# Kernel optimization log

Hardware: AMD Instinct MI355X
Metric: run time of the kernel (lower is better)

Reference implementation:

```python
import jax, jax.numpy as jnp
import numpy as np

HEADS = 4
DIM_HEAD = 128
HIDDEN = HEADS * DIM_HEAD  # 512
DIM = 256
EMBED = 256


def mish(x):
    return x * jnp.tanh(jax.nn.softplus(x))


def setup_inputs() -> dict:
    key = jax.random.key(0)
    k = jax.random.split(key, 7)
    b, a, f, t = 64, 8, DIM, 256
    x = jax.random.normal(k[0], (b, a, f, t), dtype=jnp.float32)
    time = jax.random.normal(k[1], (b, a, EMBED), dtype=jnp.float32)
    # to_qkv: Conv2d(dim, 3*hidden, 1, bias=False) -> weight [3*hidden, dim]
    w_qkv = jax.random.normal(k[2], (3 * HIDDEN, DIM), dtype=jnp.float32) * (1.0 / np.sqrt(DIM))
    # time_mlp: Mish -> Linear(embed, 3*hidden)
    w_time = jax.random.normal(k[3], (3 * HIDDEN, EMBED), dtype=jnp.float32) * (1.0 / np.sqrt(EMBED))
    b_time = jax.random.normal(k[4], (3 * HIDDEN,), dtype=jnp.float32) * 0.01
    # to_out: Conv2d(hidden, dim, 1) with bias
    w_out = jax.random.normal(k[5], (DIM, HIDDEN), dtype=jnp.float32) * (1.0 / np.sqrt(HIDDEN))
    b_out = jax.random.normal(k[6], (DIM,), dtype=jnp.float32) * 0.01
    return {"x": x, "time": time, "w_qkv": w_qkv, "w_time": w_time,
            "b_time": b_time, "w_out": w_out, "b_out": b_out}


def reference(x, time, w_qkv, w_time, b_time, w_out, b_out):
    b, a, f, t = x.shape
    heads, c = HEADS, DIM_HEAD
    # x: b a f t -> b f a t (channels-first for 1x1 conv)
    xp = jnp.transpose(x, (0, 2, 1, 3))  # [b, f, a, t]
    # 1x1 conv == channel GEMM
    qkv = jnp.einsum('of,bfat->boat', w_qkv, xp)  # [b, 3*hidden, a, t]
    # time MLP: Mish -> Linear; bias broadcast over t
    temb = mish(time) @ w_time.T + b_time          # [b, a, 3*hidden]
    temb = jnp.transpose(temb, (0, 2, 1))[..., None]  # [b, 3*hidden, a, 1]
    qkv = qkv + temb
    # 'b (qkv heads c) h w -> qkv (b h) heads c w' with h=a, w=t
    qkv = qkv.reshape(b, 3, heads, c, a, t)
    qkv = jnp.transpose(qkv, (1, 0, 4, 2, 3, 5)).reshape(3, b * a, heads, c, t)
    q, k, v = qkv[0], qkv[1], qkv[2]  # each [(b a), heads, c, t]
    k = jax.nn.softmax(k, axis=-1)
    # linear attention: context over keys/values, then apply to q
    context = jnp.einsum('bhdn,bhen->bhde', k, v)   # [(b a), heads, c, c]
    out = jnp.einsum('bhde,bhdn->bhen', context, q)  # [(b a), heads, c, t]
    # '(b h) heads c w -> b (heads c) h w'
    out = out.reshape(b, a, heads * c, t)
    out = jnp.transpose(out, (0, 2, 1, 3))  # [b, hidden, a, t]
    out = jnp.einsum('of,bfat->boat', w_out, out) + b_out[None, :, None, None]
    # b f a t -> b a f t
    return jnp.transpose(out, (0, 2, 1, 3))
```

## Files before the change

### kernel.cpp

```cpp
#include <hip/hip_runtime.h>

typedef __bf16 bf16;
typedef __bf16 bf16x4 __attribute__((ext_vector_type(4)));
typedef __bf16 bf16x8 __attribute__((ext_vector_type(8)));
typedef float  f32x4  __attribute__((ext_vector_type(4)));

#define TT    256
#define FF    256
#define SG    256
#define NGRP  2

static __device__ inline f32x4 mfma16(bf16x8 a, bf16x8 b, f32x4 c) {
    return __builtin_amdgcn_mfma_f32_16x16x32_bf16(a, b, c, 0, 0, 0);
}

typedef const __attribute__((address_space(1))) unsigned int* gp_t;
typedef __attribute__((address_space(3))) unsigned int* lp_t;
static __device__ inline void gll16(const bf16* g, bf16* l) {
    __builtin_amdgcn_global_load_lds((gp_t)g, (lp_t)l, 16, 0, 0);
}

static __device__ inline void stage128g(const bf16* __restrict__ g, int ld, bf16* __restrict__ l) {
    int lane = threadIdx.x & 63, wv = threadIdx.x >> 6;
    int r = lane >> 2, c8 = (lane & 3) * 8;
#pragma unroll
    for (int i = 0; i < 2; i++) {
        int row0 = wv * 32 + i * 16;
        gll16(g + (size_t)(row0 + r) * ld + c8, l + row0 * 32);
    }
}
static __device__ inline void stage256g(const bf16* __restrict__ g, int ld, bf16* __restrict__ l) {
    int lane = threadIdx.x & 63, wv = threadIdx.x >> 6;
    int r = lane >> 2, c8 = (lane & 3) * 8;
#pragma unroll
    for (int i = 0; i < 4; i++) {
        int row0 = wv * 64 + i * 16;
        gll16(g + (size_t)(row0 + r) * ld + c8, l + row0 * 32);
    }
}
static __device__ inline bf16x8 fragld(const bf16* __restrict__ l, int row0) {
    int lane = threadIdx.x & 63;
    return *(const bf16x8*)(l + (row0 + (lane & 15)) * 32 + (lane >> 4) * 8);
}
static __device__ inline bf16x8 fragld_s(const bf16* __restrict__ l, int row0, int stride) {
    int lane = threadIdx.x & 63;
    return *(const bf16x8*)(l + (row0 + (lane & 15)) * stride + (lane >> 4) * 8);
}

__global__ __launch_bounds__(256) void k_cvt(const float4* __restrict__ src, bf16* __restrict__ dst) {
    int i = blockIdx.x * 256 + threadIdx.x;
    float4 v = src[i];
    bf16x4 o;
    o[0] = (__bf16)v.x; o[1] = (__bf16)v.y; o[2] = (__bf16)v.z; o[3] = (__bf16)v.w;
    *(bf16x4*)(dst + (size_t)i * 4) = o;
}

__global__ __launch_bounds__(256) void k_mish(const float4* __restrict__ src, bf16* __restrict__ dst) {
    int i = blockIdx.x * 256 + threadIdx.x;
    float4 v = src[i];
    float in[4] = {v.x, v.y, v.z, v.w};
    bf16x4 o;
#pragma unroll
    for (int j = 0; j < 4; j++) {
        float sp = log1pf(__expf(in[j]));
        o[j] = (__bf16)(in[j] * tanhf(sp));
    }
    *(bf16x4*)(dst + (size_t)i * 4) = o;
}

__global__ __launch_bounds__(256) void k_xpose(const float* __restrict__ x, bf16* __restrict__ xT) {
    __shared__ float tile[64][65];
    int bid = blockIdx.x;
    int s  = bid >> 4;
    int f0 = ((bid >> 2) & 3) * 64;
    int t0 = (bid & 3) * 64;
    int tid = threadIdx.x;
    int rr = tid >> 4;
    int cc = (tid & 15) * 4;
    const float* xp = x + ((size_t)(s * FF + f0)) * TT + t0;
#pragma unroll
    for (int i = 0; i < 4; i++) {
        int r = i * 16 + rr;
        float4 v = *(const float4*)(xp + (size_t)r * TT + cc);
        tile[r][cc] = v.x; tile[r][cc + 1] = v.y; tile[r][cc + 2] = v.z; tile[r][cc + 3] = v.w;
    }
    __syncthreads();
    bf16* op = xT + ((size_t)(s * TT + t0)) * FF + f0;
#pragma unroll
    for (int i = 0; i < 4; i++) {
        int tr = i * 16 + rr;
        bf16x4 o;
        o[0] = (__bf16)tile[cc][tr];     o[1] = (__bf16)tile[cc + 1][tr];
        o[2] = (__bf16)tile[cc + 2][tr]; o[3] = (__bf16)tile[cc + 3][tr];
        *(bf16x4*)(op + (size_t)tr * FF + cc) = o;
    }
}

__global__ __launch_bounds__(256) void k_temb(const bf16* __restrict__ wt, const bf16* __restrict__ mish,
                                              const float* __restrict__ bt, float* __restrict__ tembT) {
    __shared__ bf16 lA[128 * 32];
    __shared__ bf16 lB[128 * 32];
    int o0 = blockIdx.x * 128, s0 = blockIdx.y * 128;
    int tid = threadIdx.x, wv = tid >> 6, lane = tid & 63, qd = lane >> 4, c = lane & 15;
    f32x4 acc[2][8] = {};
    for (int k0 = 0; k0 < 256; k0 += 32) {
        __syncthreads();
        stage128g(wt + (size_t)o0 * 256 + k0, 256, lA);
        stage128g(mish + (size_t)s0 * 256 + k0, 256, lB);
        __syncthreads();
        bf16x8 a0 = fragld(lA, wv * 32), a1 = fragld(lA, wv * 32 + 16);
#pragma unroll
        for (int nt = 0; nt < 8; nt++) {
            bf16x8 b = fragld(lB, nt * 16);
            acc[0][nt] = mfma16(a0, b, acc[0][nt]);
            acc[1][nt] = mfma16(a1, b, acc[1][nt]);
        }
    }
#pragma unroll
    for (int mt = 0; mt < 2; mt++)
#pragma unroll
        for (int nt = 0; nt < 8; nt++)
#pragma unroll
            for (int r = 0; r < 4; r++) {
                int o = o0 + wv * 32 + mt * 16 + qd * 4 + r;
                int s = s0 + nt * 16 + c;
                tembT[(size_t)o * 512 + s] = acc[mt][nt][r] + bt[o];
            }
}

__global__ __launch_bounds__(256) void k_qkv(const bf16* __restrict__ wq, const bf16* __restrict__ xT,
                                             const float* __restrict__ tembT,
                                             bf16* __restrict__ qt, bf16* __restrict__ kk, bf16* __restrict__ vv) {
    __shared__ bf16 lA[128 * 32];
    __shared__ bf16 lB[128 * 32];
    int b = blockIdx.x;
    int w = (b & 7) * (24 * SG / 8) + (b >> 3);
    int s = w / 24, j = w - s * 24;
    int oc = j >> 1, th = j & 1;
    int o0 = oc * 128, t0 = th * 128;
    int tid = threadIdx.x, wv = tid >> 6, lane = tid & 63, qd = lane >> 4, c = lane & 15;
    const bf16* xs = xT + (size_t)s * (TT * FF) + (size_t)t0 * FF;
    f32x4 acc[2][8] = {};
    for (int k0 = 0; k0 < 256; k0 += 32) {
        __syncthreads();
        stage128g(wq + (size_t)o0 * 256 + k0, 256, lA);
        stage128g(xs + k0, 256, lB);
        __syncthreads();
        bf16x8 a0 = fragld(lA, wv * 32), a1 = fragld(lA, wv * 32 + 16);
#pragma unroll
        for (int nt = 0; nt < 8; nt++) {
            bf16x8 bfr = fragld(lB, nt * 16);
            acc[0][nt] = mfma16(a0, bfr, acc[0][nt]);
            acc[1][nt] = mfma16(a1, bfr, acc[1][nt]);
        }
    }
    int sec = oc >> 2, h = oc & 3;
    float tb[2][4];
#pragma unroll
    for (int mt = 0; mt < 2; mt++)
#pragma unroll
        for (int r = 0; r < 4; r++)
            tb[mt][r] = tembT[(size_t)(o0 + wv * 32 + mt * 16 + qd * 4 + r) * 512 + s];
    if (sec == 0) {
#pragma unroll
        for (int mt = 0; mt < 2; mt++)
#pragma unroll
            for (int nt = 0; nt < 8; nt++) {
                int t = t0 + nt * 16 + c, dl = wv * 32 + mt * 16 + qd * 4;
                bf16x4 o;
#pragma unroll
                for (int r = 0; r < 4; r++) o[r] = (__bf16)(acc[mt][nt][r] + tb[mt][r]);
                *(bf16x4*)(qt + (((size_t)s * 4 + h) * 256 + t) * 128 + dl) = o;
            }
    } else {
        bf16* dst0 = (sec == 1 ? kk : vv);
#pragma unroll
        for (int mt = 0; mt < 2; mt++)
#pragma unroll
            for (int nt = 0; nt < 8; nt++) {
                int t = t0 + nt * 16 + c, dl = wv * 32 + mt * 16 + qd * 4;
                bf16* d = dst0 + (((size_t)s * 4 + h) * 128 + dl) * 256 + t;
#pragma unroll
                for (int r = 0; r < 4; r++) d[(size_t)r * 256] = (__bf16)(acc[mt][nt][r] + tb[mt][r]);
            }
    }
}

__global__ __launch_bounds__(256) void k_attn(const bf16* __restrict__ kk, const bf16* __restrict__ vv,
                                              const bf16* __restrict__ qt, bf16* __restrict__ midT) {
    __shared__ __align__(16) char smem[52224];
    float* mx = (float*)smem;
    float* rs = mx + 128;
    bf16* lA  = (bf16*)(smem + 1024);
    bf16* lB  = (bf16*)(smem + 1024 + 8192);
    bf16* lQ  = (bf16*)(smem + 1024);
    bf16* lct = (bf16*)(smem + 1024 + 16384);
    int bid = blockIdx.x;
    int s = bid >> 2, h = bid & 3;
    size_t base = ((size_t)s * 4 + h) * 32768;
    const bf16* kb = kk + base;
    const bf16* vb = vv + base;
    int tid = threadIdx.x, wv = tid >> 6, lane = tid & 63, qd = lane >> 4, c = lane & 15;

    {
        int d = tid >> 1, half = tid & 1;
        const bf16* p = kb + (size_t)d * 256 + half * 128;
        float m = -3e38f, l = 0.f;
#pragma unroll
        for (int ci = 0; ci < 16; ci++) {
            bf16x8 v8 = *(const bf16x8*)(p + ci * 8);
            float xv[8]; float cm = -3e38f;
#pragma unroll
            for (int j = 0; j < 8; j++) { xv[j] = (float)v8[j]; cm = fmaxf(cm, xv[j]); }
            if (cm > m) { l *= __expf(m - cm); m = cm; }
#pragma unroll
            for (int j = 0; j < 8; j++) l += __expf(xv[j] - m);
        }
        float mo = __shfl_xor(m, 1);
        float lo = __shfl_xor(l, 1);
        float M = fmaxf(m, mo);
        float L = l * __expf(m - M) + lo * __expf(mo - M);
        if (half == 0) { mx[d] = M; rs[d] = 1.0f / L; }
    }
    __syncthreads();

    f32x4 cacc[2][8] = {};
    for (int k0 = 0; k0 < 256; k0 += 32) {
        __syncthreads();
        stage128g(vb + k0, 256, lA);
        stage128g(kb + k0, 256, lB);
        __syncthreads();
        bf16x8 a0 = fragld(lA, wv * 32), a1 = fragld(lA, wv * 32 + 16);
#pragma unroll
        for (int nt = 0; nt < 8; nt++) {
            bf16x8 kf = fragld(lB, nt * 16);
            float md = mx[nt * 16 + c];
            bf16x8 b;
#pragma unroll
            for (int j = 0; j < 8; j++) b[j] = (__bf16)__expf((float)kf[j] - md);
            cacc[0][nt] = mfma16(a0, b, cacc[0][nt]);
            cacc[1][nt] = mfma16(a1, b, cacc[1][nt]);
        }
    }
    __syncthreads();
#pragma unroll
    for (int mt = 0; mt < 2; mt++)
#pragma unroll
        for (int nt = 0; nt < 8; nt++) {
            int d = nt * 16 + c;
            float rv = rs[d];
#pragma unroll
            for (int r = 0; r < 4; r++) {
                int e = wv * 32 + mt * 16 + qd * 4 + r;
                lct[e * 136 + d] = (__bf16)(cacc[mt][nt][r] * rv);
            }
        }
    __syncthreads();
    const bf16* qb = qt + base;
    for (int th = 0; th < 2; th++) {
        f32x4 oacc[2][8] = {};
        for (int d0 = 0; d0 < 128; d0 += 32) {
            __syncthreads();
            stage128g(qb + (size_t)th * 128 * 128 + d0, 128, lQ);
            __syncthreads();
            bf16x8 a0 = fragld_s(lct + d0, wv * 32, 136), a1 = fragld_s(lct + d0, wv * 32 + 16, 136);
#pragma unroll
            for (int nt = 0; nt < 8; nt++) {
                bf16x8 qf = fragld(lQ, nt * 16);
                oacc[0][nt] = mfma16(a0, qf, oacc[0][nt]);
                oacc[1][nt] = mfma16(a1, qf, oacc[1][nt]);
            }
        }
#pragma unroll
        for (int mt = 0; mt < 2; mt++)
#pragma unroll
            for (int nt = 0; nt < 8; nt++) {
                int t = th * 128 + nt * 16 + c;
                int e = wv * 32 + mt * 16 + qd * 4;
                bf16x4 o;
#pragma unroll
                for (int r = 0; r < 4; r++) o[r] = (__bf16)oacc[mt][nt][r];
                *(bf16x4*)(midT + ((size_t)s * 256 + t) * 512 + h * 128 + e) = o;
            }
    }
}

__global__ __launch_bounds__(256) void k_out(const bf16* __restrict__ wo, const bf16* __restrict__ midT,
                                             const float* __restrict__ bo, float* __restrict__ y) {
    __shared__ bf16 lA[128 * 32];
    __shared__ bf16 lB[128 * 32];
    int b = blockIdx.x;
    int w = (b & 7) * (4 * SG / 8) + (b >> 3);
    int s = w >> 2, j = w & 3;
    int o0 = (j >> 1) * 128, t0 = (j & 1) * 128;
    int tid = threadIdx.x, wv = tid >> 6, lane = tid & 63, qd = lane >> 4, c = lane & 15;
    const bf16* ms = midT + (size_t)s * 131072 + (size_t)t0 * 512;
    f32x4 acc[2][8] = {};
    for (int k0 = 0; k0 < 512; k0 += 32) {
        __syncthreads();
        stage128g(wo + (size_t)o0 * 512 + k0, 512, lA);
        stage128g(ms + k0, 512, lB);
        __syncthreads();
        bf16x8 a0 = fragld(lA, wv * 32), a1 = fragld(lA, wv * 32 + 16);
#pragma unroll
        for (int nt = 0; nt < 8; nt++) {
            bf16x8 bfr = fragld(lB, nt * 16);
            acc[0][nt] = mfma16(a0, bfr, acc[0][nt]);
            acc[1][nt] = mfma16(a1, bfr, acc[1][nt]);
        }
    }
    float bb[2][4];
#pragma unroll
    for (int mt = 0; mt < 2; mt++)
#pragma unroll
        for (int r = 0; r < 4; r++)
            bb[mt][r] = bo[o0 + wv * 32 + mt * 16 + qd * 4 + r];
#pragma unroll
    for (int mt = 0; mt < 2; mt++)
#pragma unroll
        for (int nt = 0; nt < 8; nt++)
#pragma unroll
            for (int r = 0; r < 4; r++) {
                int o = o0 + wv * 32 + mt * 16 + qd * 4 + r;
                int t = t0 + nt * 16 + c;
                y[((size_t)(s * 256 + o)) * 256 + t] = acc[mt][nt][r] + bb[mt][r];
            }
}

extern "C" void kernel_launch(void* const* d_in, const int* in_sizes, int n_in,
                              void* d_out, int out_size, void* d_ws, size_t ws_size,
                              hipStream_t stream) {
    const float* x      = (const float*)d_in[0];
    const float* time_  = (const float*)d_in[1];
    const float* w_qkv  = (const float*)d_in[2];
    const float* w_time = (const float*)d_in[3];
    const float* b_time = (const float*)d_in[4];
    const float* w_out  = (const float*)d_in[5];
    const float* b_out  = (const float*)d_in[6];
    float* y = (float*)d_out;
    char* ws = (char*)d_ws;

    bf16*  wqkv_bf  = (bf16*)(ws + 0);
    bf16*  wtime_bf = (bf16*)(ws + 786432);
    bf16*  wout_bf  = (bf16*)(ws + 1572864);
    bf16*  mish_bf  = (bf16*)(ws + 1835008);
    float* tembT    = (float*)(ws + 2097152);
    bf16*  qt       = (bf16*)(ws + 5242880);
    bf16*  kk       = (bf16*)(ws + 72351744);
    bf16*  vv       = (bf16*)(ws + 139460608);
    bf16*  midT     = (bf16*)(ws + 206569472);
    bf16*  xT       = (bf16*)(ws + 206569472);

    k_cvt<<<384, 256, 0, stream>>>((const float4*)w_qkv, wqkv_bf);
    k_cvt<<<384, 256, 0, stream>>>((const float4*)w_time, wtime_bf);
    k_cvt<<<128, 256, 0, stream>>>((const float4*)w_out, wout_bf);
    k_mish<<<128, 256, 0, stream>>>((const float4*)time_, mish_bf);
    k_temb<<<dim3(12, 4), 256, 0, stream>>>(wtime_bf, mish_bf, b_time, tembT);

    for (int g = 0; g < NGRP; g++) {
        const float* xg = x + (size_t)g * SG * FF * TT;
        float*       yg = y + (size_t)g * SG * 256 * TT;
        const float* tg = tembT + (size_t)g * SG;
        k_xpose<<<SG * 16, 256, 0, stream>>>(xg, xT);
        k_qkv<<<24 * SG, 256, 0, stream>>>(wqkv_bf, xT, tg, qt, kk, vv);
        k_attn<<<SG * 4, 256, 0, stream>>>(kk, vv, qt, midT);
        k_out<<<4 * SG, 256, 0, stream>>>(wout_bf, midT, b_out, yg);
    }
}
```

Measured before the change: 634.7 us.

## Double-buffer LDS tiles to overlap global loads with MFMA in all GEMMs

Converts the single-buffered LDS staging in k_temb, k_qkv, k_attn and k_out to ping-pong buffers. The next K-slice is issued with global_load_lds before computing on the current one. This leaves one barrier per iteration instead of two and hides load latency behind MFMA work. In k_attn the first V/K tiles are prefetched during the softmax-statistics pass, and Q tiles are prefetched across the th/d0 loops. The cost is doubled LDS per block (k_attn grows to about 67 KB), which can reduce how many blocks fit on a CU. The unused stage256g helper is removed.

```diff
diff --git a/kernel.cpp b/kernel.cpp
--- a/kernel.cpp
+++ b/kernel.cpp
@@ -26,15 +26,6 @@
 #pragma unroll
     for (int i = 0; i < 2; i++) {
         int row0 = wv * 32 + i * 16;
-        gll16(g + (size_t)(row0 + r) * ld + c8, l + row0 * 32);
-    }
-}
-static __device__ inline void stage256g(const bf16* __restrict__ g, int ld, bf16* __restrict__ l) {
-    int lane = threadIdx.x & 63, wv = threadIdx.x >> 6;
-    int r = lane >> 2, c8 = (lane & 3) * 8;
-#pragma unroll
-    for (int i = 0; i < 4; i++) {
-        int row0 = wv * 64 + i * 16;
         gll16(g + (size_t)(row0 + r) * ld + c8, l + row0 * 32);
     }
 }
@@ -98,23 +89,29 @@
 
 __global__ __launch_bounds__(256) void k_temb(const bf16* __restrict__ wt, const bf16* __restrict__ mish,
                                               const float* __restrict__ bt, float* __restrict__ tembT) {
-    __shared__ bf16 lA[128 * 32];
-    __shared__ bf16 lB[128 * 32];
+    __shared__ bf16 lA[2][128 * 32];
+    __shared__ bf16 lB[2][128 * 32];
     int o0 = blockIdx.x * 128, s0 = blockIdx.y * 128;
     int tid = threadIdx.x, wv = tid >> 6, lane = tid & 63, qd = lane >> 4, c = lane & 15;
     f32x4 acc[2][8] = {};
+    stage128g(wt + (size_t)o0 * 256, 256, lA[0]);
+    stage128g(mish + (size_t)s0 * 256, 256, lB[0]);
+    __syncthreads();
+    int cur = 0;
     for (int k0 = 0; k0 < 256; k0 += 32) {
-        __syncthreads();
-        stage128g(wt + (size_t)o0 * 256 + k0, 256, lA);
-        stage128g(mish + (size_t)s0 * 256 + k0, 256, lB);
-        __syncthreads();
-        bf16x8 a0 = fragld(lA, wv * 32), a1 = fragld(lA, wv * 32 + 16);
-#pragma unroll
-        for (int nt = 0; nt < 8; nt++) {
-            bf16x8 b = fragld(lB, nt * 16);
+        if (k0 + 32 < 256) {
+            stage128g(wt + (size_t)o0 * 256 + k0 + 32, 256, lA[cur ^ 1]);
+            stage128g(mish + (size_t)s0 * 256 + k0 + 32, 256, lB[cur ^ 1]);
+        }
+        bf16x8 a0 = fragld(lA[cur], wv * 32), a1 = fragld(lA[cur], wv * 32 + 16);
+#pragma unroll
+        for (int nt = 0; nt < 8; nt++) {
+            bf16x8 b = fragld(lB[cur], nt * 16);
             acc[0][nt] = mfma16(a0, b, acc[0][nt]);
             acc[1][nt] = mfma16(a1, b, acc[1][nt]);
         }
+        __syncthreads();
+        cur ^= 1;
     }
 #pragma unroll
     for (int mt = 0; mt < 2; mt++)
@@ -131,8 +128,8 @@
 __global__ __launch_bounds__(256) void k_qkv(const bf16* __restrict__ wq, const bf16* __restrict__ xT,
                                              const float* __restrict__ tembT,
                                              bf16* __restrict__ qt, bf16* __restrict__ kk, bf16* __restrict__ vv) {
-    __shared__ bf16 lA[128 * 32];
-    __shared__ bf16 lB[128 * 32];
+    __shared__ bf16 lA[2][128 * 32];
+    __shared__ bf16 lB[2][128 * 32];
     int b = blockIdx.x;
     int w = (b & 7) * (24 * SG / 8) + (b >> 3);
     int s = w / 24, j = w - s * 24;
@@ -141,18 +138,24 @@
     int tid = threadIdx.x, wv = tid >> 6, lane = tid & 63, qd = lane >> 4, c = lane & 15;
     const bf16* xs = xT + (size_t)s * (TT * FF) + (size_t)t0 * FF;
     f32x4 acc[2][8] = {};
+    stage128g(wq + (size_t)o0 * 256, 256, lA[0]);
+    stage128g(xs, 256, lB[0]);
+    __syncthreads();
+    int cur = 0;
     for (int k0 = 0; k0 < 256; k0 += 32) {
-        __syncthreads();
-        stage128g(wq + (size_t)o0 * 256 + k0, 256, lA);
-        stage128g(xs + k0, 256, lB);
-        __syncthreads();
-        bf16x8 a0 = fragld(lA, wv * 32), a1 = fragld(lA, wv * 32 + 16);
-#pragma unroll
-        for (int nt = 0; nt < 8; nt++) {
-            bf16x8 bfr = fragld(lB, nt * 16);
+        if (k0 + 32 < 256) {
+            stage128g(wq + (size_t)o0 * 256 + k0 + 32, 256, lA[cur ^ 1]);
+            stage128g(xs + k0 + 32, 256, lB[cur ^ 1]);
+        }
+        bf16x8 a0 = fragld(lA[cur], wv * 32), a1 = fragld(lA[cur], wv * 32 + 16);
+#pragma unroll
+        for (int nt = 0; nt < 8; nt++) {
+            bf16x8 bfr = fragld(lB[cur], nt * 16);
             acc[0][nt] = mfma16(a0, bfr, acc[0][nt]);
             acc[1][nt] = mfma16(a1, bfr, acc[1][nt]);
         }
+        __syncthreads();
+        cur ^= 1;
     }
     int sec = oc >> 2, h = oc & 3;
     float tb[2][4];
@@ -186,15 +189,15 @@
     }
 }
 
+#define SM_LA2(i) ((bf16*)(smem + 1024 + (size_t)(i) * 8192))
+#define SM_LB2(i) ((bf16*)(smem + 1024 + 16384 + (size_t)(i) * 8192))
+#define SM_LQ(i)  ((bf16*)(smem + 1024 + (size_t)(i) * 8192))
 __global__ __launch_bounds__(256) void k_attn(const bf16* __restrict__ kk, const bf16* __restrict__ vv,
                                               const bf16* __restrict__ qt, bf16* __restrict__ midT) {
-    __shared__ __align__(16) char smem[52224];
+    __shared__ __align__(16) char smem[68608];
     float* mx = (float*)smem;
     float* rs = mx + 128;
-    bf16* lA  = (bf16*)(smem + 1024);
-    bf16* lB  = (bf16*)(smem + 1024 + 8192);
-    bf16* lQ  = (bf16*)(smem + 1024);
-    bf16* lct = (bf16*)(smem + 1024 + 16384);
+    bf16* lct = (bf16*)(smem + 1024 + 32768);
     int bid = blockIdx.x;
     int s = bid >> 2, h = bid & 3;
     size_t base = ((size_t)s * 4 + h) * 32768;
@@ -202,6 +205,9 @@
     const bf16* vb = vv + base;
     int tid = threadIdx.x, wv = tid >> 6, lane = tid & 63, qd = lane >> 4, c = lane & 15;
 
+    stage128g(vb, 256, SM_LA2(0));
+    stage128g(kb, 256, SM_LB2(0));
+
     {
         int d = tid >> 1, half = tid & 1;
         const bf16* p = kb + (size_t)d * 256 + half * 128;
@@ -225,15 +231,16 @@
     __syncthreads();
 
     f32x4 cacc[2][8] = {};
+    int cur = 0;
     for (int k0 = 0; k0 < 256; k0 += 32) {
-        __syncthreads();
-        stage128g(vb + k0, 256, lA);
-        stage128g(kb + k0, 256, lB);
-        __syncthreads();
-        bf16x8 a0 = fragld(lA, wv * 32), a1 = fragld(lA, wv * 32 + 16);
-#pragma unroll
-        for (int nt = 0; nt < 8; nt++) {
-            bf16x8 kf = fragld(lB, nt * 16);
+        if (k0 + 32 < 256) {
+            stage128g(vb + k0 + 32, 256, SM_LA2(cur ^ 1));
+            stage128g(kb + k0 + 32, 256, SM_LB2(cur ^ 1));
+        }
+        bf16x8 a0 = fragld(SM_LA2(cur), wv * 32), a1 = fragld(SM_LA2(cur), wv * 32 + 16);
+#pragma unroll
+        for (int nt = 0; nt < 8; nt++) {
+            bf16x8 kf = fragld(SM_LB2(cur), nt * 16);
             float md = mx[nt * 16 + c];
             bf16x8 b;
 #pragma unroll
@@ -241,8 +248,13 @@
             cacc[0][nt] = mfma16(a0, b, cacc[0][nt]);
             cacc[1][nt] = mfma16(a1, b, cacc[1][nt]);
         }
-    }
-    __syncthreads();
+        __syncthreads();
+        cur ^= 1;
+    }
+
+    const bf16* qb = qt + base;
+    stage128g(qb, 128, SM_LQ(0));
+
 #pragma unroll
     for (int mt = 0; mt < 2; mt++)
 #pragma unroll
@@ -256,20 +268,25 @@
             }
         }
     __syncthreads();
-    const bf16* qb = qt + base;
+
+    cur = 0;
     for (int th = 0; th < 2; th++) {
         f32x4 oacc[2][8] = {};
         for (int d0 = 0; d0 < 128; d0 += 32) {
-            __syncthreads();
-            stage128g(qb + (size_t)th * 128 * 128 + d0, 128, lQ);
-            __syncthreads();
+            int idx = th * 4 + (d0 >> 5);
+            if (idx < 7) {
+                int n = idx + 1, th2 = n >> 2, d02 = (n & 3) * 32;
+                stage128g(qb + (size_t)th2 * 128 * 128 + d02, 128, SM_LQ(cur ^ 1));
+            }
             bf16x8 a0 = fragld_s(lct + d0, wv * 32, 136), a1 = fragld_s(lct + d0, wv * 32 + 16, 136);
 #pragma unroll
             for (int nt = 0; nt < 8; nt++) {
-                bf16x8 qf = fragld(lQ, nt * 16);
+                bf16x8 qf = fragld(SM_LQ(cur), nt * 16);
                 oacc[0][nt] = mfma16(a0, qf, oacc[0][nt]);
                 oacc[1][nt] = mfma16(a1, qf, oacc[1][nt]);
             }
+            __syncthreads();
+            cur ^= 1;
         }
 #pragma unroll
         for (int mt = 0; mt < 2; mt++)
@@ -287,8 +304,8 @@
 
 __global__ __launch_bounds__(256) void k_out(const bf16* __restrict__ wo, const bf16* __restrict__ midT,
                                              const float* __restrict__ bo, float* __restrict__ y) {
-    __shared__ bf16 lA[128 * 32];
-    __shared__ bf16 lB[128 * 32];
+    __shared__ bf16 lA[2][128 * 32];
+    __shared__ bf16 lB[2][128 * 32];
     int b = blockIdx.x;
     int w = (b & 7) * (4 * SG / 8) + (b >> 3);
     int s = w >> 2, j = w & 3;
@@ -296,18 +313,24 @@
     int tid = threadIdx.x, wv = tid >> 6, lane = tid & 63, qd = lane >> 4, c = lane & 15;
     const bf16* ms = midT + (size_t)s * 131072 + (size_t)t0 * 512;
     f32x4 acc[2][8] = {};
+    stage128g(wo + (size_t)o0 * 512, 512, lA[0]);
+    stage128g(ms, 512, lB[0]);
+    __syncthreads();
+    int cur = 0;
     for (int k0 = 0; k0 < 512; k0 += 32) {
-        __syncthreads();
-        stage128g(wo + (size_t)o0 * 512 + k0, 512, lA);
-        stage128g(ms + k0, 512, lB);
-        __syncthreads();
-        bf16x8 a0 = fragld(lA, wv * 32), a1 = fragld(lA, wv * 32 + 16);
-#pragma unroll
-        for (int nt = 0; nt < 8; nt++) {
-            bf16x8 bfr = fragld(lB, nt * 16);
+        if (k0 + 32 < 512) {
+            stage128g(wo + (size_t)o0 * 512 + k0 + 32, 512, lA[cur ^ 1]);
+            stage128g(ms + k0 + 32, 512, lB[cur ^ 1]);
+        }
+        bf16x8 a0 = fragld(lA[cur], wv * 32), a1 = fragld(lA[cur], wv * 32 + 16);
+#pragma unroll
+        for (int nt = 0; nt < 8; nt++) {
+            bf16x8 bfr = fragld(lB[cur], nt * 16);
             acc[0][nt] = mfma16(a0, bfr, acc[0][nt]);
             acc[1][nt] = mfma16(a1, bfr, acc[1][nt]);
         }
+        __syncthreads();
+        cur ^= 1;
     }
     float bb[2][4];
 #pragma unroll
```

Result: no change. 646.8 us (+1.9%).

## Double-buffer LDS staging with async global_load_lds prefetch in GEMM kernels

Applied to the files above, without the earlier changes.

Converts the K-loops of the qkv, attention and output kernels from single-buffered LDS staging with two __syncthreads per step into a two-stage ping-pong pipeline. Tiles for step t+2 are issued with global_load_lds right after step t is consumed, and each step waits on partial vmcnt counts. The goal is to hide global-load latency behind MFMA work. In the attention kernel, the first K/V tiles are also prefetched during the softmax-stats pass, and the Q tiles are prefetched while the context is written to LDS. The cost is more LDS per block, which can lower occupancy, and hand-tuned waitcnt values that are fragile if the load counts change.

```diff
diff --git a/kernel.cpp b/kernel.cpp
--- a/kernel.cpp
+++ b/kernel.cpp
@@ -10,6 +10,11 @@
 #define SG    256
 #define NGRP  2
 
+#define SCHED0 __builtin_amdgcn_sched_barrier(0)
+#define BAR    __builtin_amdgcn_s_barrier()
+#define WAITVM(N) asm volatile("s_waitcnt vmcnt(" #N ")" ::: "memory")
+#define WAITLGKM0 asm volatile("s_waitcnt lgkmcnt(0)" ::: "memory")
+
 static __device__ inline f32x4 mfma16(bf16x8 a, bf16x8 b, f32x4 c) {
     return __builtin_amdgcn_mfma_f32_16x16x32_bf16(a, b, c, 0, 0, 0);
 }
@@ -26,15 +31,6 @@
 #pragma unroll
     for (int i = 0; i < 2; i++) {
         int row0 = wv * 32 + i * 16;
-        gll16(g + (size_t)(row0 + r) * ld + c8, l + row0 * 32);
-    }
-}
-static __device__ inline void stage256g(const bf16* __restrict__ g, int ld, bf16* __restrict__ l) {
-    int lane = threadIdx.x & 63, wv = threadIdx.x >> 6;
-    int r = lane >> 2, c8 = (lane & 3) * 8;
-#pragma unroll
-    for (int i = 0; i < 4; i++) {
-        int row0 = wv * 64 + i * 16;
         gll16(g + (size_t)(row0 + r) * ld + c8, l + row0 * 32);
     }
 }
@@ -131,28 +127,40 @@
 __global__ __launch_bounds__(256) void k_qkv(const bf16* __restrict__ wq, const bf16* __restrict__ xT,
                                              const float* __restrict__ tembT,
                                              bf16* __restrict__ qt, bf16* __restrict__ kk, bf16* __restrict__ vv) {
-    __shared__ bf16 lA[128 * 32];
-    __shared__ bf16 lB[128 * 32];
+    __shared__ bf16 lA[2][128 * 32];
+    __shared__ bf16 lB[2][128 * 32];
     int b = blockIdx.x;
     int w = (b & 7) * (24 * SG / 8) + (b >> 3);
     int s = w / 24, j = w - s * 24;
     int oc = j >> 1, th = j & 1;
     int o0 = oc * 128, t0 = th * 128;
     int tid = threadIdx.x, wv = tid >> 6, lane = tid & 63, qd = lane >> 4, c = lane & 15;
+    const bf16* wA = wq + (size_t)o0 * 256;
     const bf16* xs = xT + (size_t)s * (TT * FF) + (size_t)t0 * FF;
     f32x4 acc[2][8] = {};
-    for (int k0 = 0; k0 < 256; k0 += 32) {
-        __syncthreads();
-        stage128g(wq + (size_t)o0 * 256 + k0, 256, lA);
-        stage128g(xs + k0, 256, lB);
-        __syncthreads();
-        bf16x8 a0 = fragld(lA, wv * 32), a1 = fragld(lA, wv * 32 + 16);
+    stage128g(wA, 256, lA[0]);
+    stage128g(xs, 256, lB[0]);
+    SCHED0;
+    stage128g(wA + 32, 256, lA[1]);
+    stage128g(xs + 32, 256, lB[1]);
+    SCHED0;
+#pragma unroll
+    for (int t = 0; t < 8; t++) {
+        if (t == 7) { WAITVM(0); } else { WAITVM(4); }
+        SCHED0; BAR; SCHED0;
+        bf16x8 a0 = fragld(lA[t & 1], wv * 32), a1 = fragld(lA[t & 1], wv * 32 + 16);
 #pragma unroll
         for (int nt = 0; nt < 8; nt++) {
-            bf16x8 bfr = fragld(lB, nt * 16);
+            bf16x8 bfr = fragld(lB[t & 1], nt * 16);
             acc[0][nt] = mfma16(a0, bfr, acc[0][nt]);
             acc[1][nt] = mfma16(a1, bfr, acc[1][nt]);
         }
+        SCHED0; BAR; SCHED0;
+        if (t + 2 < 8) {
+            stage128g(wA + (t + 2) * 32, 256, lA[t & 1]);
+            stage128g(xs + (t + 2) * 32, 256, lB[t & 1]);
+        }
+        SCHED0;
     }
     int sec = oc >> 2, h = oc & 3;
     float tb[2][4];
@@ -186,15 +194,15 @@
     }
 }
 
+#define SM_LA2(i) ((bf16*)(smem + 1024 + (size_t)(i) * 8192))
+#define SM_LB2(i) ((bf16*)(smem + 1024 + 16384 + (size_t)(i) * 8192))
+#define SM_LQ(i)  ((bf16*)(smem + 1024 + (size_t)(i) * 8192))
 __global__ __launch_bounds__(256) void k_attn(const bf16* __restrict__ kk, const bf16* __restrict__ vv,
                                               const bf16* __restrict__ qt, bf16* __restrict__ midT) {
-    __shared__ __align__(16) char smem[52224];
+    __shared__ __align__(16) char smem[68608];
     float* mx = (float*)smem;
     float* rs = mx + 128;
-    bf16* lA  = (bf16*)(smem + 1024);
-    bf16* lB  = (bf16*)(smem + 1024 + 8192);
-    bf16* lQ  = (bf16*)(smem + 1024);
-    bf16* lct = (bf16*)(smem + 1024 + 16384);
+    bf16* lct = (bf16*)(smem + 1024 + 32768);
     int bid = blockIdx.x;
     int s = bid >> 2, h = bid & 3;
     size_t base = ((size_t)s * 4 + h) * 32768;
@@ -202,6 +210,13 @@
     const bf16* vb = vv + base;
     int tid = threadIdx.x, wv = tid >> 6, lane = tid & 63, qd = lane >> 4, c = lane & 15;
 
+    stage128g(vb, 256, SM_LA2(0));
+    stage128g(kb, 256, SM_LB2(0));
+    SCHED0;
+    stage128g(vb + 32, 256, SM_LA2(1));
+    stage128g(kb + 32, 256, SM_LB2(1));
+    SCHED0;
+
     {
         int d = tid >> 1, half = tid & 1;
         const bf16* p = kb + (size_t)d * 256 + half * 128;
@@ -225,24 +240,35 @@
     __syncthreads();
 
     f32x4 cacc[2][8] = {};
-    for (int k0 = 0; k0 < 256; k0 += 32) {
-        __syncthreads();
-        stage128g(vb + k0, 256, lA);
-        stage128g(kb + k0, 256, lB);
-        __syncthreads();
-        bf16x8 a0 = fragld(lA, wv * 32), a1 = fragld(lA, wv * 32 + 16);
+#pragma unroll
+    for (int t = 0; t < 8; t++) {
+        if (t == 7) { WAITVM(0); } else { WAITVM(4); }
+        SCHED0; BAR; SCHED0;
+        bf16x8 a0 = fragld(SM_LA2(t & 1), wv * 32), a1 = fragld(SM_LA2(t & 1), wv * 32 + 16);
 #pragma unroll
         for (int nt = 0; nt < 8; nt++) {
-            bf16x8 kf = fragld(lB, nt * 16);
+            bf16x8 kf = fragld(SM_LB2(t & 1), nt * 16);
             float md = mx[nt * 16 + c];
-            bf16x8 b;
-#pragma unroll
-            for (int j = 0; j < 8; j++) b[j] = (__bf16)__expf((float)kf[j] - md);
-            cacc[0][nt] = mfma16(a0, b, cacc[0][nt]);
-            cacc[1][nt] = mfma16(a1, b, cacc[1][nt]);
-        }
-    }
-    __syncthreads();
+            bf16x8 bb;
+#pragma unroll
+            for (int j = 0; j < 8; j++) bb[j] = (__bf16)__expf((float)kf[j] - md);
+            cacc[0][nt] = mfma16(a0, bb, cacc[0][nt]);
+            cacc[1][nt] = mfma16(a1, bb, cacc[1][nt]);
+        }
+        SCHED0; BAR; SCHED0;
+        if (t + 2 < 8) {
+            stage128g(vb + (t + 2) * 32, 256, SM_LA2(t & 1));
+            stage128g(kb + (t + 2) * 32, 256, SM_LB2(t & 1));
+        }
+        SCHED0;
+    }
+
+    const bf16* qb = qt + base;
+    stage128g(qb, 128, SM_LQ(0));
+    SCHED0;
+    stage128g(qb + 32, 128, SM_LQ(1));
+    SCHED0;
+
 #pragma unroll
     for (int mt = 0; mt < 2; mt++)
 #pragma unroll
@@ -255,21 +281,33 @@
                 lct[e * 136 + d] = (__bf16)(cacc[mt][nt][r] * rv);
             }
         }
-    __syncthreads();
-    const bf16* qb = qt + base;
+    WAITLGKM0;
+    SCHED0; BAR; SCHED0;
+
+#pragma unroll
     for (int th = 0; th < 2; th++) {
         f32x4 oacc[2][8] = {};
-        for (int d0 = 0; d0 < 128; d0 += 32) {
-            __syncthreads();
-            stage128g(qb + (size_t)th * 128 * 128 + d0, 128, lQ);
-            __syncthreads();
+#pragma unroll
+        for (int dd = 0; dd < 4; dd++) {
+            int idx = th * 4 + dd;
+            int d0 = dd * 32;
+            if (idx == 7)                    { WAITVM(0); }
+            else if (idx == 4 || idx == 5)   { WAITVM(16); }
+            else                             { WAITVM(2); }
+            SCHED0; BAR; SCHED0;
             bf16x8 a0 = fragld_s(lct + d0, wv * 32, 136), a1 = fragld_s(lct + d0, wv * 32 + 16, 136);
 #pragma unroll
             for (int nt = 0; nt < 8; nt++) {
-                bf16x8 qf = fragld(lQ, nt * 16);
+                bf16x8 qf = fragld(SM_LQ(idx & 1), nt * 16);
                 oacc[0][nt] = mfma16(a0, qf, oacc[0][nt]);
                 oacc[1][nt] = mfma16(a1, qf, oacc[1][nt]);
             }
+            SCHED0; BAR; SCHED0;
+            if (idx + 2 < 8) {
+                int n = idx + 2;
+                stage128g(qb + (size_t)(n >> 2) * 16384 + (n & 3) * 32, 128, SM_LQ(idx & 1));
+            }
+            SCHED0;
         }
 #pragma unroll
         for (int mt = 0; mt < 2; mt++)
@@ -287,27 +325,39 @@
 
 __global__ __launch_bounds__(256) void k_out(const bf16* __restrict__ wo, const bf16* __restrict__ midT,
                                              const float* __restrict__ bo, float* __restrict__ y) {
-    __shared__ bf16 lA[128 * 32];
-    __shared__ bf16 lB[128 * 32];
+    __shared__ bf16 lA[2][128 * 32];
+    __shared__ bf16 lB[2][128 * 32];
     int b = blockIdx.x;
     int w = (b & 7) * (4 * SG / 8) + (b >> 3);
     int s = w >> 2, j = w & 3;
     int o0 = (j >> 1) * 128, t0 = (j & 1) * 128;
     int tid = threadIdx.x, wv = tid >> 6, lane = tid & 63, qd = lane >> 4, c = lane & 15;
+    const bf16* wA = wo + (size_t)o0 * 512;
     const bf16* ms = midT + (size_t)s * 131072 + (size_t)t0 * 512;
     f32x4 acc[2][8] = {};
-    for (int k0 = 0; k0 < 512; k0 += 32) {
-        __syncthreads();
-        stage128g(wo + (size_t)o0 * 512 + k0, 512, lA);
-        stage128g(ms + k0, 512, lB);
-        __syncthreads();
-        bf16x8 a0 = fragld(lA, wv * 32), a1 = fragld(lA, wv * 32 + 16);
+    stage128g(wA, 512, lA[0]);
+    stage128g(ms, 512, lB[0]);
+    SCHED0;
+    stage128g(wA + 32, 512, lA[1]);
+    stage128g(ms + 32, 512, lB[1]);
+    SCHED0;
+#pragma unroll
+    for (int t = 0; t < 16; t++) {
+        if (t == 15) { WAITVM(0); } else { WAITVM(4); }
+        SCHED0; BAR; SCHED0;
+        bf16x8 a0 = fragld(lA[t & 1], wv * 32), a1 = fragld(lA[t & 1], wv * 32 + 16);
 #pragma unroll
         for (int nt = 0; nt < 8; nt++) {
-            bf16x8 bfr = fragld(lB, nt * 16);
+            bf16x8 bfr = fragld(lB[t & 1], nt * 16);
             acc[0][nt] = mfma16(a0, bfr, acc[0][nt]);
             acc[1][nt] = mfma16(a1, bfr, acc[1][nt]);
         }
+        SCHED0; BAR; SCHED0;
+        if (t + 2 < 16) {
+            stage128g(wA + (t + 2) * 32, 512, lA[t & 1]);
+            stage128g(ms + (t + 2) * 32, 512, lB[t & 1]);
+        }
+        SCHED0;
     }
     float bb[2][4];
 #pragma unroll
```

After: 616.6 us. 2.9% less time.

## Fuse QKV projection with linear attention and double-buffer output GEMM

Applied to the files above, without the earlier changes.

Merges the QKV projection and attention kernels into one 512-thread kernel per (sample, head). It computes K and V per 128-token half into LDS, runs an online softmax across the halves, then recomputes Q and applies the context, so the large q/k/v intermediates never go to global memory. The output projection GEMM also gains double-buffered LDS staging with explicit vmcnt waits. The costs are a large LDS footprint that limits occupancy, only 1024 blocks for the fused kernel, and x being reloaded for the Q pass.

```diff
diff --git a/kernel.cpp b/kernel.cpp
--- a/kernel.cpp
+++ b/kernel.cpp
@@ -10,6 +10,10 @@
 #define SG    256
 #define NGRP  2
 
+#define SCHED0 __builtin_amdgcn_sched_barrier(0)
+#define BAR    __builtin_amdgcn_s_barrier()
+#define WAITVM(N) asm volatile("s_waitcnt vmcnt(" #N ")" ::: "memory")
+
 static __device__ inline f32x4 mfma16(bf16x8 a, bf16x8 b, f32x4 c) {
     return __builtin_amdgcn_mfma_f32_16x16x32_bf16(a, b, c, 0, 0, 0);
 }
@@ -29,14 +33,11 @@
         gll16(g + (size_t)(row0 + r) * ld + c8, l + row0 * 32);
     }
 }
-static __device__ inline void stage256g(const bf16* __restrict__ g, int ld, bf16* __restrict__ l) {
+static __device__ inline void stage8(const bf16* __restrict__ g, int ld, bf16* __restrict__ l) {
     int lane = threadIdx.x & 63, wv = threadIdx.x >> 6;
     int r = lane >> 2, c8 = (lane & 3) * 8;
-#pragma unroll
-    for (int i = 0; i < 4; i++) {
-        int row0 = wv * 64 + i * 16;
-        gll16(g + (size_t)(row0 + r) * ld + c8, l + row0 * 32);
-    }
+    int row0 = wv * 16;
+    gll16(g + (size_t)(row0 + r) * ld + c8, l + row0 * 32);
 }
 static __device__ inline bf16x8 fragld(const bf16* __restrict__ l, int row0) {
     int lane = threadIdx.x & 63;
@@ -128,186 +129,218 @@
             }
 }
 
-__global__ __launch_bounds__(256) void k_qkv(const bf16* __restrict__ wq, const bf16* __restrict__ xT,
-                                             const float* __restrict__ tembT,
-                                             bf16* __restrict__ qt, bf16* __restrict__ kk, bf16* __restrict__ vv) {
-    __shared__ bf16 lA[128 * 32];
-    __shared__ bf16 lB[128 * 32];
+__global__ __launch_bounds__(512) void k_fused(const bf16* __restrict__ wqkv, const bf16* __restrict__ xT,
+                                               const float* __restrict__ tembT, bf16* __restrict__ midT) {
+    __shared__ __align__(16) char smem[124928];
+    bf16*  lx  = (bf16*)(smem);
+    bf16*  lwA = (bf16*)(smem + 8192);
+    bf16*  lwB = (bf16*)(smem + 16384);
+    float* mx  = (float*)(smem + 24576);
+    float* ls  = (float*)(smem + 25088);
+    float* rs  = (float*)(smem + 25600);
+    float* rfb = (float*)(smem + 26112);
+    bf16*  lk  = (bf16*)(smem + 26624);
+    bf16*  lv  = (bf16*)(smem + 59392);
+    bf16*  lq  = (bf16*)(smem + 92160);
+    bf16*  lct = (bf16*)(smem + 26624);
+
     int b = blockIdx.x;
-    int w = (b & 7) * (24 * SG / 8) + (b >> 3);
-    int s = w / 24, j = w - s * 24;
-    int oc = j >> 1, th = j & 1;
-    int o0 = oc * 128, t0 = th * 128;
+    int w = (b & 7) * (4 * SG / 8) + (b >> 3);
+    int s = w >> 2, h = w & 3;
     int tid = threadIdx.x, wv = tid >> 6, lane = tid & 63, qd = lane >> 4, c = lane & 15;
-    const bf16* xs = xT + (size_t)s * (TT * FF) + (size_t)t0 * FF;
-    f32x4 acc[2][8] = {};
-    for (int k0 = 0; k0 < 256; k0 += 32) {
-        __syncthreads();
-        stage128g(wq + (size_t)o0 * 256 + k0, 256, lA);
-        stage128g(xs + k0, 256, lB);
-        __syncthreads();
-        bf16x8 a0 = fragld(lA, wv * 32), a1 = fragld(lA, wv * 32 + 16);
+    const bf16* xs = xT + (size_t)s * (TT * FF);
+    const bf16* Wq = wqkv + (size_t)(h * 128) * 256;
+    const bf16* Wk = wqkv + (size_t)(512 + h * 128) * 256;
+    const bf16* Wv = wqkv + (size_t)(1024 + h * 128) * 256;
+
+    f32x4 cacc[8] = {};
+
+    for (int th = 0; th < 2; th++) {
+        f32x4 kacc[8] = {}, vacc[8] = {};
+        const bf16* xh = xs + (size_t)th * 128 * 256;
+        for (int f0 = 0; f0 < 256; f0 += 32) {
+            __syncthreads();
+            stage8(xh + f0, 256, lx);
+            stage8(Wk + f0, 256, lwA);
+            stage8(Wv + f0, 256, lwB);
+            __syncthreads();
+            bf16x8 a0 = fragld(lx, wv * 16);
+#pragma unroll
+            for (int nt = 0; nt < 8; nt++) {
+                kacc[nt] = mfma16(a0, fragld(lwA, nt * 16), kacc[nt]);
+                vacc[nt] = mfma16(a0, fragld(lwB, nt * 16), vacc[nt]);
+            }
+        }
+        {
+            float tbk[8], tbv[8];
+#pragma unroll
+            for (int nt = 0; nt < 8; nt++) {
+                tbk[nt] = tembT[(size_t)(512 + h * 128 + nt * 16 + c) * 512 + s];
+                tbv[nt] = tembT[(size_t)(1024 + h * 128 + nt * 16 + c) * 512 + s];
+            }
+            int addr0 = (wv >> 1) * 4096 + (wv & 1) * 16 + qd * 4;
+#pragma unroll
+            for (int nt = 0; nt < 8; nt++) {
+                bf16x4 ok, ov;
+#pragma unroll
+                for (int r = 0; r < 4; r++) {
+                    ok[r] = (__bf16)(kacc[nt][r] + tbk[nt]);
+                    ov[r] = (__bf16)(vacc[nt][r] + tbv[nt]);
+                }
+                int ad = addr0 + (nt * 16 + c) * 32;
+                *(bf16x4*)(lk + ad) = ok;
+                *(bf16x4*)(lv + ad) = ov;
+            }
+        }
+        __syncthreads();
+        {
+            int d = tid >> 2, q4 = tid & 3;
+            const bf16* p = lk + q4 * 4096 + d * 32;
+            float m = -3e38f, l = 0.f;
+#pragma unroll
+            for (int ci = 0; ci < 4; ci++) {
+                bf16x8 v8 = *(const bf16x8*)(p + ci * 8);
+                float xv[8]; float cm = -3e38f;
+#pragma unroll
+                for (int j2 = 0; j2 < 8; j2++) { xv[j2] = (float)v8[j2]; cm = fmaxf(cm, xv[j2]); }
+                if (cm > m) { l *= __expf(m - cm); m = cm; }
+#pragma unroll
+                for (int j2 = 0; j2 < 8; j2++) l += __expf(xv[j2] - m);
+            }
+            float mo = __shfl_xor(m, 1), lo = __shfl_xor(l, 1);
+            float M = fmaxf(m, mo); l = l * __expf(m - M) + lo * __expf(mo - M); m = M;
+            mo = __shfl_xor(m, 2); lo = __shfl_xor(l, 2);
+            M = fmaxf(m, mo); l = l * __expf(m - M) + lo * __expf(mo - M); m = M;
+            if (q4 == 0) {
+                if (th == 0) { mx[d] = m; ls[d] = l; }
+                else {
+                    float Mo = mx[d];
+                    float M2 = fmaxf(Mo, m);
+                    float rf = __expf(Mo - M2);
+                    float L  = ls[d] * rf + l * __expf(m - M2);
+                    mx[d] = M2; rs[d] = 1.0f / L; rfb[d] = rf;
+                }
+            }
+        }
+        __syncthreads();
+        if (th == 1) {
+#pragma unroll
+            for (int nt = 0; nt < 8; nt++) {
+                float rf = rfb[nt * 16 + c];
+#pragma unroll
+                for (int r = 0; r < 4; r++) cacc[nt][r] *= rf;
+            }
+        }
+#pragma unroll
+        for (int tc = 0; tc < 4; tc++) {
+            bf16x8 a0 = fragld(lv + tc * 4096, wv * 16);
+#pragma unroll
+            for (int nt = 0; nt < 8; nt++) {
+                bf16x8 kf = fragld(lk + tc * 4096, nt * 16);
+                float md = mx[nt * 16 + c];
+                bf16x8 bb;
+#pragma unroll
+                for (int j2 = 0; j2 < 8; j2++) bb[j2] = (__bf16)__expf((float)kf[j2] - md);
+                cacc[nt] = mfma16(a0, bb, cacc[nt]);
+            }
+        }
+        __syncthreads();
+    }
+
+#pragma unroll
+    for (int nt = 0; nt < 8; nt++) {
+        int d = nt * 16 + c;
+        float rv = rs[d];
+#pragma unroll
+        for (int r = 0; r < 4; r++)
+            lct[(wv * 16 + qd * 4 + r) * 136 + d] = (__bf16)(cacc[nt][r] * rv);
+    }
+    __syncthreads();
+
+    for (int th = 0; th < 2; th++) {
+        f32x4 qacc[8] = {};
+        const bf16* xh = xs + (size_t)th * 128 * 256;
+        for (int f0 = 0; f0 < 256; f0 += 32) {
+            __syncthreads();
+            stage8(xh + f0, 256, lx);
+            stage8(Wq + f0, 256, lwA);
+            __syncthreads();
+            bf16x8 a0 = fragld(lwA, wv * 16);
+#pragma unroll
+            for (int nt = 0; nt < 8; nt++)
+                qacc[nt] = mfma16(a0, fragld(lx, nt * 16), qacc[nt]);
+        }
+        {
+            float tbq[4];
+#pragma unroll
+            for (int r = 0; r < 4; r++)
+                tbq[r] = tembT[(size_t)(h * 128 + wv * 16 + qd * 4 + r) * 512 + s];
+            int addr0 = (wv >> 1) * 4096 + (wv & 1) * 16 + qd * 4;
+#pragma unroll
+            for (int nt = 0; nt < 8; nt++) {
+                bf16x4 oq;
+#pragma unroll
+                for (int r = 0; r < 4; r++) oq[r] = (__bf16)(qacc[nt][r] + tbq[r]);
+                *(bf16x4*)(lq + addr0 + (nt * 16 + c) * 32) = oq;
+            }
+        }
+        __syncthreads();
+        f32x4 oacc[8] = {};
+#pragma unroll
+        for (int dc = 0; dc < 4; dc++) {
+            bf16x8 a0 = fragld_s(lct + dc * 32, wv * 16, 136);
+#pragma unroll
+            for (int nt = 0; nt < 8; nt++)
+                oacc[nt] = mfma16(a0, fragld(lq + dc * 4096, nt * 16), oacc[nt]);
+        }
 #pragma unroll
         for (int nt = 0; nt < 8; nt++) {
-            bf16x8 bfr = fragld(lB, nt * 16);
-            acc[0][nt] = mfma16(a0, bfr, acc[0][nt]);
-            acc[1][nt] = mfma16(a1, bfr, acc[1][nt]);
-        }
-    }
-    int sec = oc >> 2, h = oc & 3;
-    float tb[2][4];
-#pragma unroll
-    for (int mt = 0; mt < 2; mt++)
-#pragma unroll
-        for (int r = 0; r < 4; r++)
-            tb[mt][r] = tembT[(size_t)(o0 + wv * 32 + mt * 16 + qd * 4 + r) * 512 + s];
-    if (sec == 0) {
-#pragma unroll
-        for (int mt = 0; mt < 2; mt++)
-#pragma unroll
-            for (int nt = 0; nt < 8; nt++) {
-                int t = t0 + nt * 16 + c, dl = wv * 32 + mt * 16 + qd * 4;
-                bf16x4 o;
-#pragma unroll
-                for (int r = 0; r < 4; r++) o[r] = (__bf16)(acc[mt][nt][r] + tb[mt][r]);
-                *(bf16x4*)(qt + (((size_t)s * 4 + h) * 256 + t) * 128 + dl) = o;
-            }
-    } else {
-        bf16* dst0 = (sec == 1 ? kk : vv);
-#pragma unroll
-        for (int mt = 0; mt < 2; mt++)
-#pragma unroll
-            for (int nt = 0; nt < 8; nt++) {
-                int t = t0 + nt * 16 + c, dl = wv * 32 + mt * 16 + qd * 4;
-                bf16* d = dst0 + (((size_t)s * 4 + h) * 128 + dl) * 256 + t;
-#pragma unroll
-                for (int r = 0; r < 4; r++) d[(size_t)r * 256] = (__bf16)(acc[mt][nt][r] + tb[mt][r]);
-            }
-    }
-}
-
-__global__ __launch_bounds__(256) void k_attn(const bf16* __restrict__ kk, const bf16* __restrict__ vv,
-                                              const bf16* __restrict__ qt, bf16* __restrict__ midT) {
-    __shared__ __align__(16) char smem[52224];
-    float* mx = (float*)smem;
-    float* rs = mx + 128;
-    bf16* lA  = (bf16*)(smem + 1024);
-    bf16* lB  = (bf16*)(smem + 1024 + 8192);
-    bf16* lQ  = (bf16*)(smem + 1024);
-    bf16* lct = (bf16*)(smem + 1024 + 16384);
-    int bid = blockIdx.x;
-    int s = bid >> 2, h = bid & 3;
-    size_t base = ((size_t)s * 4 + h) * 32768;
-    const bf16* kb = kk + base;
-    const bf16* vb = vv + base;
-    int tid = threadIdx.x, wv = tid >> 6, lane = tid & 63, qd = lane >> 4, c = lane & 15;
-
-    {
-        int d = tid >> 1, half = tid & 1;
-        const bf16* p = kb + (size_t)d * 256 + half * 128;
-        float m = -3e38f, l = 0.f;
-#pragma unroll
-        for (int ci = 0; ci < 16; ci++) {
-            bf16x8 v8 = *(const bf16x8*)(p + ci * 8);
-            float xv[8]; float cm = -3e38f;
-#pragma unroll
-            for (int j = 0; j < 8; j++) { xv[j] = (float)v8[j]; cm = fmaxf(cm, xv[j]); }
-            if (cm > m) { l *= __expf(m - cm); m = cm; }
-#pragma unroll
-            for (int j = 0; j < 8; j++) l += __expf(xv[j] - m);
-        }
-        float mo = __shfl_xor(m, 1);
-        float lo = __shfl_xor(l, 1);
-        float M = fmaxf(m, mo);
-        float L = l * __expf(m - M) + lo * __expf(mo - M);
-        if (half == 0) { mx[d] = M; rs[d] = 1.0f / L; }
-    }
-    __syncthreads();
-
-    f32x4 cacc[2][8] = {};
-    for (int k0 = 0; k0 < 256; k0 += 32) {
-        __syncthreads();
-        stage128g(vb + k0, 256, lA);
-        stage128g(kb + k0, 256, lB);
-        __syncthreads();
-        bf16x8 a0 = fragld(lA, wv * 32), a1 = fragld(lA, wv * 32 + 16);
-#pragma unroll
-        for (int nt = 0; nt < 8; nt++) {
-            bf16x8 kf = fragld(lB, nt * 16);
-            float md = mx[nt * 16 + c];
-            bf16x8 b;
-#pragma unroll
-            for (int j = 0; j < 8; j++) b[j] = (__bf16)__expf((float)kf[j] - md);
-            cacc[0][nt] = mfma16(a0, b, cacc[0][nt]);
-            cacc[1][nt] = mfma16(a1, b, cacc[1][nt]);
-        }
-    }
-    __syncthreads();
-#pragma unroll
-    for (int mt = 0; mt < 2; mt++)
-#pragma unroll
-        for (int nt = 0; nt < 8; nt++) {
-            int d = nt * 16 + c;
-            float rv = rs[d];
-#pragma unroll
-            for (int r = 0; r < 4; r++) {
-                int e = wv * 32 + mt * 16 + qd * 4 + r;
-                lct[e * 136 + d] = (__bf16)(cacc[mt][nt][r] * rv);
-            }
-        }
-    __syncthreads();
-    const bf16* qb = qt + base;
-    for (int th = 0; th < 2; th++) {
-        f32x4 oacc[2][8] = {};
-        for (int d0 = 0; d0 < 128; d0 += 32) {
-            __syncthreads();
-            stage128g(qb + (size_t)th * 128 * 128 + d0, 128, lQ);
-            __syncthreads();
-            bf16x8 a0 = fragld_s(lct + d0, wv * 32, 136), a1 = fragld_s(lct + d0, wv * 32 + 16, 136);
-#pragma unroll
-            for (int nt = 0; nt < 8; nt++) {
-                bf16x8 qf = fragld(lQ, nt * 16);
-                oacc[0][nt] = mfma16(a0, qf, oacc[0][nt]);
-                oacc[1][nt] = mfma16(a1, qf, oacc[1][nt]);
-            }
-        }
-#pragma unroll
-        for (int mt = 0; mt < 2; mt++)
-#pragma unroll
-            for (int nt = 0; nt < 8; nt++) {
-                int t = th * 128 + nt * 16 + c;
-                int e = wv * 32 + mt * 16 + qd * 4;
-                bf16x4 o;
-#pragma unroll
-                for (int r = 0; r < 4; r++) o[r] = (__bf16)oacc[mt][nt][r];
-                *(bf16x4*)(midT + ((size_t)s * 256 + t) * 512 + h * 128 + e) = o;
-            }
+            int t = th * 128 + nt * 16 + c;
+            int e = wv * 16 + qd * 4;
+            bf16x4 o;
+#pragma unroll
+            for (int r = 0; r < 4; r++) o[r] = (__bf16)oacc[nt][r];
+            *(bf16x4*)(midT + ((size_t)s * 256 + t) * 512 + h * 128 + e) = o;
+        }
+        __syncthreads();
     }
 }
 
 __global__ __launch_bounds__(256) void k_out(const bf16* __restrict__ wo, const bf16* __restrict__ midT,
                                              const float* __restrict__ bo, float* __restrict__ y) {
-    __shared__ bf16 lA[128 * 32];
-    __shared__ bf16 lB[128 * 32];
+    __shared__ bf16 lA[2][128 * 32];
+    __shared__ bf16 lB[2][128 * 32];
     int b = blockIdx.x;
     int w = (b & 7) * (4 * SG / 8) + (b >> 3);
     int s = w >> 2, j = w & 3;
     int o0 = (j >> 1) * 128, t0 = (j & 1) * 128;
     int tid = threadIdx.x, wv = tid >> 6, lane = tid & 63, qd = lane >> 4, c = lane & 15;
+    const bf16* wA = wo + (size_t)o0 * 512;
     const bf16* ms = midT + (size_t)s * 131072 + (size_t)t0 * 512;
     f32x4 acc[2][8] = {};
-    for (int k0 = 0; k0 < 512; k0 += 32) {
-        __syncthreads();
-        stage128g(wo + (size_t)o0 * 512 + k0, 512, lA);
-        stage128g(ms + k0, 512, lB);
-        __syncthreads();
-        bf16x8 a0 = fragld(lA, wv * 32), a1 = fragld(lA, wv * 32 + 16);
+    stage128g(wA, 512, lA[0]);
+    stage128g(ms, 512, lB[0]);
+    SCHED0;
+    stage128g(wA + 32, 512, lA[1]);
+    stage128g(ms + 32, 512, lB[1]);
+    SCHED0;
+#pragma unroll
+    for (int t = 0; t < 16; t++) {
+        if (t == 15) { WAITVM(0); } else { WAITVM(4); }
+        SCHED0; BAR; SCHED0;
+        bf16x8 a0 = fragld(lA[t & 1], wv * 32), a1 = fragld(lA[t & 1], wv * 32 + 16);
 #pragma unroll
         for (int nt = 0; nt < 8; nt++) {
-            bf16x8 bfr = fragld(lB, nt * 16);
+            bf16x8 bfr = fragld(lB[t & 1], nt * 16);
             acc[0][nt] = mfma16(a0, bfr, acc[0][nt]);
             acc[1][nt] = mfma16(a1, bfr, acc[1][nt]);
         }
+        SCHED0; BAR; SCHED0;
+        if (t + 2 < 16) {
+            stage128g(wA + (t + 2) * 32, 512, lA[t & 1]);
+            stage128g(ms + (t + 2) * 32, 512, lB[t & 1]);
+        }
+        SCHED0;
     }
     float bb[2][4];
 #pragma unroll
@@ -345,11 +378,8 @@
     bf16*  wout_bf  = (bf16*)(ws + 1572864);
     bf16*  mish_bf  = (bf16*)(ws + 1835008);
     float* tembT    = (float*)(ws + 2097152);
-    bf16*  qt       = (bf16*)(ws + 5242880);
-    bf16*  kk       = (bf16*)(ws + 72351744);
-    bf16*  vv       = (bf16*)(ws + 139460608);
+    bf16*  xT       = (bf16*)(ws + 5242880);
     bf16*  midT     = (bf16*)(ws + 206569472);
-    bf16*  xT       = (bf16*)(ws + 206569472);
 
     k_cvt<<<384, 256, 0, stream>>>((const float4*)w_qkv, wqkv_bf);
     k_cvt<<<384, 256, 0, stream>>>((const float4*)w_time, wtime_bf);
@@ -362,8 +392,7 @@
         float*       yg = y + (size_t)g * SG * 256 * TT;
         const float* tg = tembT + (size_t)g * SG;
         k_xpose<<<SG * 16, 256, 0, stream>>>(xg, xT);
-        k_qkv<<<24 * SG, 256, 0, stream>>>(wqkv_bf, xT, tg, qt, kk, vv);
-        k_attn<<<SG * 4, 256, 0, stream>>>(kk, vv, qt, midT);
+        k_fused<<<SG * 4, 512, 0, stream>>>(wqkv_bf, xT, tg, midT);
         k_out<<<4 * SG, 256, 0, stream>>>(wout_bf, midT, b_out, yg);
     }
 }
```

Result: slower. 712.5 us (+12.2%).
